# Kernel optimization log

Measured on AMD Instinct MI355X. Metric: run time of the kernel, lower is better.

Reference implementation:

```python
import jax, jax.numpy as jnp
import numpy as np

N_NODES = 50000  # n_diseases + n_drugs
N_EDGES = 800000
DIM = 64
N_HOPS = 3


def setup_inputs() -> dict:
    key = jax.random.key(0)
    k1, k2, k3, k4 = jax.random.split(key, 4)
    embed = jax.random.normal(k1, (N_NODES, DIM), dtype=jnp.float32)
    row = jax.random.randint(k2, (N_EDGES,), 0, N_NODES)
    col = jax.random.randint(k3, (N_EDGES,), 0, N_NODES)
    edge_index = jnp.stack([row, col]).astype(jnp.int64)
    trend = jax.random.uniform(k4, (N_EDGES,), dtype=jnp.float32)
    return {"embed": embed, "edge_index": edge_index, "trend": trend}


def reference(embed, edge_index, trend):
    # GraphConv_CA: repeated gather(row) -> scale by per-edge trend -> scatter_add(col)
    n = embed.shape[0]
    row, col = edge_index[0], edge_index[1]
    t = trend[:, None]  # [E, 1]

    def hop(agg, _):
        out = agg[row] * t                                      # [E, D] gather + scale
        agg = jax.ops.segment_sum(out, col, num_segments=n)     # [N, D] scatter-add
        return agg, agg

    _, hops = jax.lax.scan(hop, embed, None, length=N_HOPS)     # [H, N, D]
    embs = jnp.concatenate([embed[:, None, :], jnp.moveaxis(hops, 0, 1)], axis=1)  # [N, H+1, D]
    return embs
```

## Files before the change

kernel.cpp:

```cpp
#include <hip/hip_runtime.h>
#include <hip/hip_fp16.h>

#define N_NODES 50000
#define N_EDGES 800000
#define DIM 64
#define OUT_STRIDE 256
#define CAP 64

#define NBUCK 196
#define BCAP 4608
#define ACHUNK 4096
#define ABLOCKS ((N_EDGES + ACHUNK - 1) / ACHUNK)
#define EMBED_F4 (N_NODES * 16)

typedef float f32x4 __attribute__((ext_vector_type(4)));

__device__ __forceinline__ long long pack_ll(int x, int y) {
    return (long long)(((unsigned long long)(unsigned)y << 32) | (unsigned)x);
}

__device__ __forceinline__ void excl_scan256(int* hist, int* scan, int tid) {
    if (tid < 256) scan[tid] = hist[tid];
    __syncthreads();
    #pragma unroll
    for (int off = 1; off < 256; off <<= 1) {
        int v = 0, u = 0;
        if (tid < 256) { v = scan[tid]; u = (tid >= off) ? scan[tid - off] : 0; }
        __syncthreads();
        if (tid < 256) scan[tid] = v + u;
        __syncthreads();
    }
    if (tid < 256) scan[tid] -= hist[tid];
    __syncthreads();
}

__global__ __launch_bounds__(512) void bucket_partition(const int* __restrict__ row,
                                                        const int* __restrict__ col,
                                                        const float* __restrict__ trend,
                                                        int* __restrict__ gcnt,
                                                        long long* __restrict__ barr) {
    __shared__ int hist[256], scan[256], cur[256], gbase[256];
    __shared__ int2 stage[ACHUNK];
    int tid = threadIdx.x;
    int e0 = blockIdx.x * ACHUNK;
    int ne = N_EDGES - e0; if (ne > ACHUNK) ne = ACHUNK;

    if (tid < 256) hist[tid] = 0;
    __syncthreads();
    for (int j = tid; j < ne; j += 512)
        atomicAdd(&hist[(unsigned)col[e0 + j] >> 8], 1);
    __syncthreads();
    excl_scan256(hist, scan, tid);
    if (tid < 256) {
        cur[tid] = scan[tid];
        gbase[tid] = (tid < NBUCK && hist[tid] > 0) ? atomicAdd(&gcnt[tid], hist[tid]) : 0;
    }
    __syncthreads();
    for (int j = tid; j < ne; j += 512) {
        int c  = col[e0 + j];
        int rr = row[e0 + j];
        float tt = trend[e0 + j];
        int bk = (unsigned)c >> 8, cl = c & 255;
        int s = atomicAdd(&cur[bk], 1);
        stage[s] = make_int2(rr | (cl << 16) | (bk << 24), __float_as_int(tt));
    }
    __syncthreads();
    for (int j = tid; j < ne; j += 512) {
        int2 v = stage[j];
        int bk = (unsigned)v.x >> 24;
        int pos = gbase[bk] + (j - scan[bk]);
        if (pos < BCAP)
            __builtin_nontemporal_store(pack_ll(v.x, v.y), &barr[bk * BCAP + pos]);
    }
}

__global__ __launch_bounds__(512) void node_sort_prep(const int* __restrict__ gcnt,
                                                      long long* __restrict__ barr,
                                                      int* __restrict__ starts,
                                                      int* __restrict__ cntc,
                                                      const float4* __restrict__ embed4,
                                                      float4* __restrict__ out4,
                                                      uint2* __restrict__ m0) {
    __shared__ int hist[256], scan[256], cur[256];
    __shared__ int2 stage[BCAP];
    int tid = threadIdx.x;
    int bk = blockIdx.x;
    int base = bk * BCAP;
    int nb = gcnt[bk]; if (nb > BCAP) nb = BCAP;

    if (tid < 256) hist[tid] = 0;
    __syncthreads();
    for (int j = tid; j < nb; j += 512) {
        long long v = barr[base + j];
        atomicAdd(&hist[((unsigned)(v & 0xFFFFFFFFu) >> 16) & 255], 1);
    }
    __syncthreads();
    excl_scan256(hist, scan, tid);
    if (tid < 256) cur[tid] = scan[tid];
    __syncthreads();
    for (int j = tid; j < nb; j += 512) {
        long long v = barr[base + j];
        int x = (int)(v & 0xFFFFFFFFu);
        int cl = ((unsigned)x >> 16) & 255;
        int s = atomicAdd(&cur[cl], 1);
        stage[s] = make_int2(x, (int)(v >> 32));
    }
    __syncthreads();
    for (int j = tid; j < nb; j += 512) {
        int2 v = stage[j];
        __builtin_nontemporal_store(pack_ll(v.x, v.y), &barr[base + j]);
    }
    if (tid < 256) {
        int node = (bk << 8) | tid;
        if (node < N_NODES) {
            starts[node] = base + scan[tid];
            int h = hist[tid]; if (h > CAP) h = CAP;
            cntc[node] = h;
        }
    }
    for (int idx = blockIdx.x * 512 + tid; idx < EMBED_F4; idx += NBUCK * 512) {
        float4 v = embed4[idx];
        int node = idx >> 4, j = idx & 15;
        f32x4 a = {v.x, v.y, v.z, v.w};
        __builtin_nontemporal_store(a, (f32x4*)&out4[node * 64 + j]);
        __half2 h01 = __floats2half2_rn(v.x, v.y);
        __half2 h23 = __floats2half2_rn(v.z, v.w);
        uint2 u;
        u.x = *(unsigned int*)&h01;
        u.y = *(unsigned int*)&h23;
        m0[(size_t)(node << 4) + j] = u;
    }
}

__global__ __launch_bounds__(256) void hop4(const int* __restrict__ starts,
                                            const int* __restrict__ cntc,
                                            const long long* __restrict__ barr,
                                            const uint2* __restrict__ msrc,
                                            float4* __restrict__ dstf,
                                            uint2* __restrict__ mdst) {
    int wave = (int)((blockIdx.x * 256 + threadIdx.x) >> 6);
    int lane = threadIdx.x & 63;
    int sub   = lane >> 4;
    int piece = lane & 15;
    int gbase = lane & 0x30;
    int node = (wave << 2) + sub;
    bool nvalid = node < N_NODES;
    int n  = nvalid ? cntc[node] : 0;
    int st = nvalid ? starts[node] : 0;

    float4 acc = make_float4(0.f, 0.f, 0.f, 0.f);
    for (int k = 0; k < n; k += 16) {
        long long pv = 0;
        int ej = k + piece;
        if (ej < n) pv = __builtin_nontemporal_load(&barr[st + ej]);
        int   r = (int)(pv & 0xFFFF);
        float t = __int_as_float((int)((unsigned long long)pv >> 32));
        int m = n - k; if (m > 16) m = 16;
        for (int j = 0; j < m; j += 4) {
            #pragma unroll
            for (int s = 0; s < 4; ++s) {
                int jj = j + s;
                int   ri = __shfl(r, gbase + jj);
                float ti = __shfl(t, gbase + jj);
                bool valid = jj < m;
                ri = valid ? ri : 0;
                ti = valid ? ti : 0.f;
                uint2 u = msrc[(size_t)(ri << 4) + piece];
                float2 f01 = __half22float2(*(__half2*)&u.x);
                float2 f23 = __half22float2(*(__half2*)&u.y);
                acc.x = fmaf(f01.x, ti, acc.x);
                acc.y = fmaf(f01.y, ti, acc.y);
                acc.z = fmaf(f23.x, ti, acc.z);
                acc.w = fmaf(f23.y, ti, acc.w);
            }
        }
    }
    if (nvalid) {
        f32x4 a = {acc.x, acc.y, acc.z, acc.w};
        __builtin_nontemporal_store(a, (f32x4*)&dstf[(size_t)node * 64 + piece]);
        if (mdst) {
            __half2 h01 = __floats2half2_rn(acc.x, acc.y);
            __half2 h23 = __floats2half2_rn(acc.z, acc.w);
            uint2 u;
            u.x = *(unsigned int*)&h01;
            u.y = *(unsigned int*)&h23;
            mdst[(size_t)(node << 4) + piece] = u;
        }
    }
}


__global__ __launch_bounds__(256) void init_out_full(const float4* __restrict__ embed4,
                                                     float4* __restrict__ out4) {
    int idx = blockIdx.x * 256 + threadIdx.x;
    if (idx >= N_NODES * 64) return;
    int node = idx >> 6;
    int j = idx & 63;
    float4 v = make_float4(0.f, 0.f, 0.f, 0.f);
    if (j < 16) v = embed4[(node << 4) + j];
    out4[idx] = v;
}

__global__ __launch_bounds__(256) void hop_atomic(const int* __restrict__ row,
                                                  const int* __restrict__ col,
                                                  const float* __restrict__ trend,
                                                  const float* __restrict__ agg_in,
                                                  float* __restrict__ agg_out) {
    int e = (int)((blockIdx.x * 256 + threadIdx.x) >> 6);
    int lane = threadIdx.x & 63;
    if (e >= N_EDGES) return;
    float v = agg_in[(size_t)row[e] * OUT_STRIDE + lane] * trend[e];
    atomicAdd(&agg_out[(size_t)col[e] * OUT_STRIDE + lane], v);
}

extern "C" void kernel_launch(void* const* d_in, const int* in_sizes, int n_in,
                              void* d_out, int out_size, void* d_ws, size_t ws_size,
                              hipStream_t stream) {
    const float* embed = (const float*)d_in[0];
    const int*   edge  = (const int*)d_in[1];
    const float* trend = (const float*)d_in[2];
    const int* row = edge;
    const int* col = edge + N_EDGES;
    float* out = (float*)d_out;
    float4* out4 = (float4*)out;

    size_t gcnt_b   = 256 * 4;
    size_t starts_b = (size_t)N_NODES * 4;
    size_t cntc_b   = (size_t)N_NODES * 4;
    size_t mirror_b = (size_t)N_NODES * DIM * 2;
    size_t barr_b   = ((size_t)NBUCK * BCAP + 64) * 8;
    size_t need = gcnt_b + starts_b + cntc_b + 2 * mirror_b + barr_b;

    if (ws_size >= need) {
        char* p = (char*)d_ws;
        int* gcnt   = (int*)p;          p += gcnt_b;
        int* starts = (int*)p;          p += starts_b;
        int* cntc   = (int*)p;          p += cntc_b;
        uint2* mA   = (uint2*)p;        p += mirror_b;
        uint2* mB   = (uint2*)p;        p += mirror_b;
        long long* barr = (long long*)p;

        hipMemsetAsync(gcnt, 0, gcnt_b, stream);

        hipLaunchKernelGGL(bucket_partition, dim3(ABLOCKS), dim3(512), 0, stream,
                           row, col, trend, gcnt, barr);
        hipLaunchKernelGGL(node_sort_prep, dim3(NBUCK), dim3(512), 0, stream,
                           gcnt, barr, starts, cntc,
                           (const float4*)embed, out4, mA);

        int hopBlocks = (N_NODES / 4 + 3) / 4 + 1;
        hopBlocks = (N_NODES + 15) / 16;
        hipLaunchKernelGGL(hop4, dim3(hopBlocks), dim3(256), 0, stream,
                           starts, cntc, barr, mA, out4 + 1 * 16, mB);
        hipLaunchKernelGGL(hop4, dim3(hopBlocks), dim3(256), 0, stream,
                           starts, cntc, barr, mB, out4 + 2 * 16, mA);
        hipLaunchKernelGGL(hop4, dim3(hopBlocks), dim3(256), 0, stream,
                           starts, cntc, barr, mA, out4 + 3 * 16, (uint2*)nullptr);
    } else {
        int initBlocks = (N_NODES * 64 + 255) / 256;
        hipLaunchKernelGGL(init_out_full, dim3(initBlocks), dim3(256), 0, stream,
                           (const float4*)embed, out4);
        int hopBlocksA = (N_EDGES * 64) / 256;
        for (int h = 1; h <= 3; ++h) {
            hipLaunchKernelGGL(hop_atomic, dim3(hopBlocksA), dim3(256), 0, stream,
                               row, col, trend, out + (h - 1) * DIM, out + h * DIM);
        }
    }
}
```

Measured before the change: 89.79 us.

## Compact edge records to 32-bit with fp16 trend and move embed init into partition

The node sort now writes a separate compact edge array in which each edge is a 32-bit word: a 16-bit source index plus the trend in fp16. The hop kernels read this array instead of the 64-bit records, which halves edge-list traffic and needs one shuffle per edge instead of two. The embed copy and the fp16 mirror initialization move from the node-sort kernel into the partition kernel, and the per-lane validity masking in the inner loop is dropped. In exchange, trend is rounded to fp16, which adds precision error, and an extra workspace buffer is required.

```diff
diff --git a/kernel.cpp b/kernel.cpp
--- a/kernel.cpp
+++ b/kernel.cpp
@@ -12,6 +12,7 @@
 #define ACHUNK 4096
 #define ABLOCKS ((N_EDGES + ACHUNK - 1) / ACHUNK)
 #define EMBED_F4 (N_NODES * 16)
+#define ATHREADS (ABLOCKS * 512)
 
 typedef float f32x4 __attribute__((ext_vector_type(4)));
 
@@ -38,7 +39,10 @@
                                                         const int* __restrict__ col,
                                                         const float* __restrict__ trend,
                                                         int* __restrict__ gcnt,
-                                                        long long* __restrict__ barr) {
+                                                        long long* __restrict__ barr,
+                                                        const float4* __restrict__ embed4,
+                                                        float4* __restrict__ out4,
+                                                        uint2* __restrict__ m0) {
     __shared__ int hist[256], scan[256], cur[256], gbase[256];
     __shared__ int2 stage[ACHUNK];
     int tid = threadIdx.x;
@@ -72,53 +76,7 @@
         if (pos < BCAP)
             __builtin_nontemporal_store(pack_ll(v.x, v.y), &barr[bk * BCAP + pos]);
     }
-}
-
-__global__ __launch_bounds__(512) void node_sort_prep(const int* __restrict__ gcnt,
-                                                      long long* __restrict__ barr,
-                                                      int* __restrict__ starts,
-                                                      int* __restrict__ cntc,
-                                                      const float4* __restrict__ embed4,
-                                                      float4* __restrict__ out4,
-                                                      uint2* __restrict__ m0) {
-    __shared__ int hist[256], scan[256], cur[256];
-    __shared__ int2 stage[BCAP];
-    int tid = threadIdx.x;
-    int bk = blockIdx.x;
-    int base = bk * BCAP;
-    int nb = gcnt[bk]; if (nb > BCAP) nb = BCAP;
-
-    if (tid < 256) hist[tid] = 0;
-    __syncthreads();
-    for (int j = tid; j < nb; j += 512) {
-        long long v = barr[base + j];
-        atomicAdd(&hist[((unsigned)(v & 0xFFFFFFFFu) >> 16) & 255], 1);
-    }
-    __syncthreads();
-    excl_scan256(hist, scan, tid);
-    if (tid < 256) cur[tid] = scan[tid];
-    __syncthreads();
-    for (int j = tid; j < nb; j += 512) {
-        long long v = barr[base + j];
-        int x = (int)(v & 0xFFFFFFFFu);
-        int cl = ((unsigned)x >> 16) & 255;
-        int s = atomicAdd(&cur[cl], 1);
-        stage[s] = make_int2(x, (int)(v >> 32));
-    }
-    __syncthreads();
-    for (int j = tid; j < nb; j += 512) {
-        int2 v = stage[j];
-        __builtin_nontemporal_store(pack_ll(v.x, v.y), &barr[base + j]);
-    }
-    if (tid < 256) {
-        int node = (bk << 8) | tid;
-        if (node < N_NODES) {
-            starts[node] = base + scan[tid];
-            int h = hist[tid]; if (h > CAP) h = CAP;
-            cntc[node] = h;
-        }
-    }
-    for (int idx = blockIdx.x * 512 + tid; idx < EMBED_F4; idx += NBUCK * 512) {
+    for (int idx = blockIdx.x * 512 + tid; idx < EMBED_F4; idx += ATHREADS) {
         float4 v = embed4[idx];
         int node = idx >> 4, j = idx & 15;
         f32x4 a = {v.x, v.y, v.z, v.w};
@@ -132,12 +90,59 @@
     }
 }
 
-__global__ __launch_bounds__(256) void hop4(const int* __restrict__ starts,
-                                            const int* __restrict__ cntc,
-                                            const long long* __restrict__ barr,
-                                            const uint2* __restrict__ msrc,
-                                            float4* __restrict__ dstf,
-                                            uint2* __restrict__ mdst) {
+__global__ __launch_bounds__(512) void node_sort_compact(const int* __restrict__ gcnt,
+                                                         const long long* __restrict__ barr,
+                                                         int* __restrict__ starts,
+                                                         int* __restrict__ cntc,
+                                                         unsigned int* __restrict__ cbarr) {
+    __shared__ int hist[256], scan[256], cur[256];
+    __shared__ int2 stage[BCAP];
+    int tid = threadIdx.x;
+    int bk = blockIdx.x;
+    int base = bk * BCAP;
+    int nb = gcnt[bk]; if (nb > BCAP) nb = BCAP;
+
+    if (tid < 256) hist[tid] = 0;
+    __syncthreads();
+    for (int j = tid; j < nb; j += 512) {
+        long long v = barr[base + j];
+        atomicAdd(&hist[((unsigned)(v & 0xFFFFFFFFu) >> 16) & 255], 1);
+    }
+    __syncthreads();
+    excl_scan256(hist, scan, tid);
+    if (tid < 256) cur[tid] = scan[tid];
+    __syncthreads();
+    for (int j = tid; j < nb; j += 512) {
+        long long v = barr[base + j];
+        int x = (int)(v & 0xFFFFFFFFu);
+        int cl = ((unsigned)x >> 16) & 255;
+        int s = atomicAdd(&cur[cl], 1);
+        stage[s] = make_int2(x, (int)(v >> 32));
+    }
+    __syncthreads();
+    for (int j = tid; j < nb; j += 512) {
+        int2 v = stage[j];
+        __half h = __float2half_rn(__int_as_float(v.y));
+        unsigned int rt = ((unsigned)v.x & 0xFFFFu)
+                        | ((unsigned)*(unsigned short*)&h << 16);
+        __builtin_nontemporal_store(rt, &cbarr[base + j]);
+    }
+    if (tid < 256) {
+        int node = (bk << 8) | tid;
+        if (node < N_NODES) {
+            starts[node] = base + scan[tid];
+            int h = hist[tid]; if (h > CAP) h = CAP;
+            cntc[node] = h;
+        }
+    }
+}
+
+__global__ __launch_bounds__(256) void hop4c(const int* __restrict__ starts,
+                                             const int* __restrict__ cntc,
+                                             const unsigned int* __restrict__ cbarr,
+                                             const uint2* __restrict__ msrc,
+                                             float4* __restrict__ dstf,
+                                             uint2* __restrict__ mdst) {
     int wave = (int)((blockIdx.x * 256 + threadIdx.x) >> 6);
     int lane = threadIdx.x & 63;
     int sub   = lane >> 4;
@@ -150,21 +155,17 @@
 
     float4 acc = make_float4(0.f, 0.f, 0.f, 0.f);
     for (int k = 0; k < n; k += 16) {
-        long long pv = 0;
+        unsigned int pv = 0;
         int ej = k + piece;
-        if (ej < n) pv = __builtin_nontemporal_load(&barr[st + ej]);
-        int   r = (int)(pv & 0xFFFF);
-        float t = __int_as_float((int)((unsigned long long)pv >> 32));
+        if (ej < n) pv = __builtin_nontemporal_load(&cbarr[st + ej]);
         int m = n - k; if (m > 16) m = 16;
         for (int j = 0; j < m; j += 4) {
             #pragma unroll
             for (int s = 0; s < 4; ++s) {
-                int jj = j + s;
-                int   ri = __shfl(r, gbase + jj);
-                float ti = __shfl(t, gbase + jj);
-                bool valid = jj < m;
-                ri = valid ? ri : 0;
-                ti = valid ? ti : 0.f;
+                unsigned int v = __shfl(pv, gbase + j + s);
+                int ri = (int)(v & 0xFFFFu);
+                unsigned short tb = (unsigned short)(v >> 16);
+                float ti = __half2float(*(__half*)&tb);
                 uint2 u = msrc[(size_t)(ri << 4) + piece];
                 float2 f01 = __half22float2(*(__half2*)&u.x);
                 float2 f23 = __half22float2(*(__half2*)&u.y);
@@ -229,7 +230,8 @@
     size_t cntc_b   = (size_t)N_NODES * 4;
     size_t mirror_b = (size_t)N_NODES * DIM * 2;
     size_t barr_b   = ((size_t)NBUCK * BCAP + 64) * 8;
-    size_t need = gcnt_b + starts_b + cntc_b + 2 * mirror_b + barr_b;
+    size_t cbarr_b  = ((size_t)NBUCK * BCAP + 64) * 4;
+    size_t need = gcnt_b + starts_b + cntc_b + 2 * mirror_b + barr_b + cbarr_b;
 
     if (ws_size >= need) {
         char* p = (char*)d_ws;
@@ -238,24 +240,24 @@
         int* cntc   = (int*)p;          p += cntc_b;
         uint2* mA   = (uint2*)p;        p += mirror_b;
         uint2* mB   = (uint2*)p;        p += mirror_b;
-        long long* barr = (long long*)p;
+        long long* barr = (long long*)p; p += barr_b;
+        unsigned int* cbarr = (unsigned int*)p;
 
         hipMemsetAsync(gcnt, 0, gcnt_b, stream);
 
         hipLaunchKernelGGL(bucket_partition, dim3(ABLOCKS), dim3(512), 0, stream,
-                           row, col, trend, gcnt, barr);
-        hipLaunchKernelGGL(node_sort_prep, dim3(NBUCK), dim3(512), 0, stream,
-                           gcnt, barr, starts, cntc,
+                           row, col, trend, gcnt, barr,
                            (const float4*)embed, out4, mA);
-
-        int hopBlocks = (N_NODES / 4 + 3) / 4 + 1;
-        hopBlocks = (N_NODES + 15) / 16;
-        hipLaunchKernelGGL(hop4, dim3(hopBlocks), dim3(256), 0, stream,
-                           starts, cntc, barr, mA, out4 + 1 * 16, mB);
-        hipLaunchKernelGGL(hop4, dim3(hopBlocks), dim3(256), 0, stream,
-                           starts, cntc, barr, mB, out4 + 2 * 16, mA);
-        hipLaunchKernelGGL(hop4, dim3(hopBlocks), dim3(256), 0, stream,
-                           starts, cntc, barr, mA, out4 + 3 * 16, (uint2*)nullptr);
+        hipLaunchKernelGGL(node_sort_compact, dim3(NBUCK), dim3(512), 0, stream,
+                           gcnt, barr, starts, cntc, cbarr);
+
+        int hopBlocks = (N_NODES + 15) / 16;
+        hipLaunchKernelGGL(hop4c, dim3(hopBlocks), dim3(256), 0, stream,
+                           starts, cntc, cbarr, mA, out4 + 1 * 16, mB);
+        hipLaunchKernelGGL(hop4c, dim3(hopBlocks), dim3(256), 0, stream,
+                           starts, cntc, cbarr, mB, out4 + 2 * 16, mA);
+        hipLaunchKernelGGL(hop4c, dim3(hopBlocks), dim3(256), 0, stream,
+                           starts, cntc, cbarr, mA, out4 + 3 * 16, (uint2*)nullptr);
     } else {
         int initBlocks = (N_NODES * 64 + 255) / 256;
         hipLaunchKernelGGL(init_out_full, dim3(initBlocks), dim3(256), 0, stream,
```

Result: faster. 87.34 us (-2.7%).
